# Kernel optimization log

Measured on AMD Instinct MI355X. Metric: run time of the kernel, lower is better.

## Reference

```python
import jax, jax.numpy as jnp
import numpy as np

N, C, NIRR, E = 2048, 128, 9, 10          # nodes, channels, sum(2l+1) of input irreps, num elements
DOUT = (1, 3)                              # output irrep dims for 128x0e + 128x1o
K3, K2, K1 = 4, 3, 2                       # number of CG paths per correlation order


def setup_inputs() -> dict:
    key = jax.random.key(0)
    ks = jax.random.split(key, 24)
    inp = {
        'node_feats': jax.random.normal(ks[0], (N, C, NIRR), jnp.float32),
        'node_attrs': jax.nn.one_hot(jax.random.randint(ks[1], (N,), 0, E), E, dtype=jnp.float32),
        'sc': jax.random.normal(ks[2], (N, C * sum(DOUT)), jnp.float32),
    }
    i = 3
    for li, d in enumerate(DOUT):
        # U tensors: fixed (buffer) generalized CG coupling tensors; sparse in e3nn,
        # here random dense stand-ins with the exact same shapes / contraction structure.
        inp[f'u3_l{li}'] = 0.1 * jax.random.normal(ks[i + 0], (d, NIRR, NIRR, NIRR, K3), jnp.float32)
        inp[f'u2_l{li}'] = 0.1 * jax.random.normal(ks[i + 1], (d, NIRR, NIRR, K2), jnp.float32)
        inp[f'u1_l{li}'] = 0.1 * jax.random.normal(ks[i + 2], (d, NIRR, K1), jnp.float32)
        s3, s2, s1 = 1.0 / np.sqrt(K3 * C), 1.0 / np.sqrt(K2 * C), 1.0 / np.sqrt(K1 * C)
        inp[f'w3_l{li}'] = s3 * jax.random.normal(ks[i + 3], (E, K3, C), jnp.float32)
        inp[f'w2_l{li}'] = s2 * jax.random.normal(ks[i + 4], (E, K2, C), jnp.float32)
        inp[f'w1_l{li}'] = s1 * jax.random.normal(ks[i + 5], (E, K1, C), jnp.float32)
        i += 6
    inp['lin_w0'] = jax.random.normal(ks[i], (C, C), jnp.float32)
    inp['lin_w1'] = jax.random.normal(ks[i + 1], (C, C), jnp.float32)
    return inp


def _contraction(x, y, u3, u2, u1, w3, w2, w1):
    # MACE Contraction: correlation-3 nested CG contraction for one output irrep.
    # x: [N,C,n], y: [N,E] one-hot, u_nu: [d, n*nu, k_nu], w_nu: [E, k_nu, C]
    wk3 = jnp.einsum('ekc,be->bkc', w3, y)                       # per-node path weights
    out = jnp.einsum('dpqik,bkc,bci->bcdpq', u3, wk3, x)         # main, nu=3
    out = jnp.einsum('dpik,ekc,be->bcdpi', u2, w2, y) + out      # add nu=2 weights
    out = jnp.einsum('bcdpi,bci->bcdp', out, x)                  # contract one feature index
    out = jnp.einsum('dik,ekc,be->bcdi', u1, w1, y) + out        # add nu=1 weights
    out = jnp.einsum('bcdi,bci->bcd', out, x)                    # [N,C,d]
    return out


def reference(node_feats, node_attrs, sc,
              u3_l0, u2_l0, u1_l0, w3_l0, w2_l0, w1_l0,
              u3_l1, u2_l1, u1_l1, w3_l1, w2_l1, w1_l1,
              lin_w0, lin_w1):
    f0 = _contraction(node_feats, node_attrs, u3_l0, u2_l0, u1_l0, w3_l0, w2_l0, w1_l0)  # [N,C,1]
    f1 = _contraction(node_feats, node_attrs, u3_l1, u2_l1, u1_l1, w3_l1, w2_l1, w1_l1)  # [N,C,3]
    inv_sqrt_c = 1.0 / np.sqrt(C).astype(np.float32)
    # o3.Linear: block-diagonal channel mixing per irrep, 1/sqrt(fan_in) normalization
    o0 = jnp.einsum('bim,ij->bjm', f0, lin_w0) * inv_sqrt_c
    o1 = jnp.einsum('bim,ij->bjm', f1, lin_w1) * inv_sqrt_c
    out = jnp.concatenate([o0.reshape(o0.shape[0], -1), o1.reshape(o1.shape[0], -1)], axis=-1)
    return out + sc
```

## Files before the change

kernel.cpp:

```cpp
#include <hip/hip_runtime.h>

#define N_NODES 2048
#define C_CH    128
#define NIRR    9
#define E_EL    10

#define NS3 165
#define NS2 45
#define US3_FLOATS (NS3 * 16)
#define US2_FLOATS (NS2 * 12)
#define US1_FLOATS (9 * 8)

struct Tab {
    unsigned char pairP[NS2], pairQ[NS2];
    unsigned char triPair[NS3], triI[NS3];
};
constexpr Tab makeTab() {
    Tab t{};
    int s2 = 0, s3 = 0;
    for (int p = 0; p < 9; p++)
        for (int q = p; q < 9; q++) {
            t.pairP[s2] = (unsigned char)p;
            t.pairQ[s2] = (unsigned char)q;
            for (int i = q; i < 9; i++) {
                t.triPair[s3] = (unsigned char)s2;
                t.triI[s3] = (unsigned char)i;
                s3++;
            }
            s2++;
        }
    return t;
}
constexpr Tab TAB = makeTab();

__global__ __launch_bounds__(256) void build_sym_kernel(
    const float* __restrict__ u3_l0, const float* __restrict__ u2_l0, const float* __restrict__ u1_l0,
    const float* __restrict__ u3_l1, const float* __restrict__ u2_l1, const float* __restrict__ u1_l1,
    float* __restrict__ us3, float* __restrict__ us2, float* __restrict__ us1)
{
    int t = blockIdx.x * 256 + threadIdx.x;
    if (t < US3_FLOATS) {
        int s = t >> 4, dk = t & 15, ds = dk >> 2, k = dk & 3;
        int pp = 0, qq = 0, ii = 0, cntr = 0;
        for (int p = 0; p < 9; p++)
            for (int q = p; q < 9; q++)
                for (int i = q; i < 9; i++) {
                    if (cntr == s) { pp = p; qq = q; ii = i; }
                    cntr++;
                }
        const float* u = (ds == 0) ? u3_l0 : (u3_l1 + (ds - 1) * 2916);
        int perm[6][3] = {{pp,qq,ii},{pp,ii,qq},{qq,pp,ii},{qq,ii,pp},{ii,pp,qq},{ii,qq,pp}};
        float acc = 0.f;
        #pragma unroll
        for (int j = 0; j < 6; j++)
            acc += u[((perm[j][0] * 9 + perm[j][1]) * 9 + perm[j][2]) * 4 + k];
        float mult = (pp == qq && qq == ii) ? 6.f : ((pp == qq || qq == ii) ? 2.f : 1.f);
        us3[ds * (NS3 * 4) + s * 4 + k] = acc / mult;
    } else if (t < US3_FLOATS + US2_FLOATS) {
        int t2 = t - US3_FLOATS;
        int s = t2 / 12, dk = t2 % 12, ds = dk / 3, k = dk % 3;
        int pp = 0, qq = 0, cntr = 0;
        for (int p = 0; p < 9; p++)
            for (int q = p; q < 9; q++) {
                if (cntr == s) { pp = p; qq = q; }
                cntr++;
            }
        const float* u = (ds == 0) ? u2_l0 : (u2_l1 + (ds - 1) * 243);
        float acc = u[(pp * 9 + qq) * 3 + k] + u[(qq * 9 + pp) * 3 + k];
        us2[ds * (NS2 * 3) + s * 3 + k] = (pp == qq) ? acc * 0.5f : acc;
    } else if (t < US3_FLOATS + US2_FLOATS + US1_FLOATS) {
        int t1 = t - US3_FLOATS - US2_FLOATS;
        int p = t1 >> 3, dk = t1 & 7, ds = dk >> 1, k = dk & 1;
        const float* u = (ds == 0) ? u1_l0 : (u1_l1 + (ds - 1) * 18);
        us1[ds * 18 + p * 2 + k] = u[p * 2 + k];
    }
}

__global__ __launch_bounds__(512, 4) void fused_kernel(
    const float* __restrict__ x, const float* __restrict__ y,
    const float* __restrict__ us3, const float* __restrict__ us2, const float* __restrict__ us1,
    const float* __restrict__ w3_l0, const float* __restrict__ w2_l0, const float* __restrict__ w1_l0,
    const float* __restrict__ w3_l1, const float* __restrict__ w2_l1, const float* __restrict__ w1_l1,
    const float* __restrict__ lw0, const float* __restrict__ lw1,
    const float* __restrict__ sc, float* __restrict__ out)
{
    __shared__ float fs[4][132];
    int tid = threadIdx.x;
    int c = tid & 127;
    int r = __builtin_amdgcn_readfirstlane(tid >> 7);
    int b = blockIdx.x;

    int e = 0;
    #pragma unroll
    for (int k = 1; k < E_EL; k++)
        if (y[b * E_EL + k] > 0.5f) e = k;
    e = __builtin_amdgcn_readfirstlane(e);

    float xv[9];
    {
        const float* xp = x + ((size_t)b * C_CH + c) * NIRR;
        #pragma unroll
        for (int i = 0; i < 9; i++) xv[i] = xp[i];
    }

    const float* t3 = us3 + r * (NS3 * 4);
    const float* t2 = us2 + r * (NS2 * 3);
    const float* t1 = us1 + r * 18;

    float G3[4] = {0.f, 0.f, 0.f, 0.f};
    float G2[3] = {0.f, 0.f, 0.f};
    float G1[2] = {0.f, 0.f};

    #pragma unroll
    for (int p = 0; p < 9; p++) {
        G1[0] += t1[p * 2 + 0] * xv[p];
        G1[1] += t1[p * 2 + 1] * xv[p];
    }

    float pq = 0.f;
    #pragma unroll
    for (int s = 0; s < NS3; s++) {
        const int pi = TAB.triPair[s];
        if (s == 0 || TAB.triPair[s] != TAB.triPair[s - 1]) {
            pq = xv[TAB.pairP[pi]] * xv[TAB.pairQ[pi]];
            G2[0] += t2[pi * 3 + 0] * pq;
            G2[1] += t2[pi * 3 + 1] * pq;
            G2[2] += t2[pi * 3 + 2] * pq;
        }
        float X = pq * xv[TAB.triI[s]];
        G3[0] += t3[s * 4 + 0] * X;
        G3[1] += t3[s * 4 + 1] * X;
        G3[2] += t3[s * 4 + 2] * X;
        G3[3] += t3[s * 4 + 3] * X;
    }

    float acc = 0.f;
    if (r == 0) {
        #pragma unroll
        for (int k = 0; k < 4; k++) acc += w3_l0[(e * 4 + k) * 128 + c] * G3[k];
        #pragma unroll
        for (int k = 0; k < 3; k++) acc += w2_l0[(e * 3 + k) * 128 + c] * G2[k];
        #pragma unroll
        for (int k = 0; k < 2; k++) acc += w1_l0[(e * 2 + k) * 128 + c] * G1[k];
    } else {
        #pragma unroll
        for (int k = 0; k < 4; k++) acc += w3_l1[(e * 4 + k) * 128 + c] * G3[k];
        #pragma unroll
        for (int k = 0; k < 3; k++) acc += w2_l1[(e * 3 + k) * 128 + c] * G2[k];
        #pragma unroll
        for (int k = 0; k < 2; k++) acc += w1_l1[(e * 2 + k) * 128 + c] * G1[k];
    }
    fs[r][c] = acc;
    __syncthreads();

    int sel, j, col;
    const float* W;
    if (tid < 128) { sel = 0; j = tid; col = tid; W = lw0; }
    else {
        int u = tid - 128;
        int m = u >> 7;
        j = u & 127;
        sel = 1 + m;
        col = 128 + 3 * j + m;
        W = lw1;
    }
    sel = __builtin_amdgcn_readfirstlane(sel);

    float a = 0.f;
    #pragma unroll 8
    for (int ib = 0; ib < 32; ib++) {
        float4 f = *(const float4*)&fs[sel][4 * ib];
        int i0 = 4 * ib;
        a += f.x * W[(i0 + 0) * 128 + j];
        a += f.y * W[(i0 + 1) * 128 + j];
        a += f.z * W[(i0 + 2) * 128 + j];
        a += f.w * W[(i0 + 3) * 128 + j];
    }

    const float inv_sqrt_c = 0.08838834764831845f;
    size_t oi = (size_t)b * 512 + col;
    out[oi] = a * inv_sqrt_c + sc[oi];
}

extern "C" void kernel_launch(void* const* d_in, const int* in_sizes, int n_in,
                              void* d_out, int out_size, void* d_ws, size_t ws_size,
                              hipStream_t stream) {
    const float* x     = (const float*)d_in[0];
    const float* y     = (const float*)d_in[1];
    const float* sc    = (const float*)d_in[2];
    const float* u3_l0 = (const float*)d_in[3];
    const float* u2_l0 = (const float*)d_in[4];
    const float* u1_l0 = (const float*)d_in[5];
    const float* w3_l0 = (const float*)d_in[6];
    const float* w2_l0 = (const float*)d_in[7];
    const float* w1_l0 = (const float*)d_in[8];
    const float* u3_l1 = (const float*)d_in[9];
    const float* u2_l1 = (const float*)d_in[10];
    const float* u1_l1 = (const float*)d_in[11];
    const float* w3_l1 = (const float*)d_in[12];
    const float* w2_l1 = (const float*)d_in[13];
    const float* w1_l1 = (const float*)d_in[14];
    const float* lw0   = (const float*)d_in[15];
    const float* lw1   = (const float*)d_in[16];
    float* out = (float*)d_out;

    float* us3 = (float*)d_ws;
    float* us2 = us3 + US3_FLOATS;
    float* us1 = us2 + US2_FLOATS;

    build_sym_kernel<<<13, 256, 0, stream>>>(
        u3_l0, u2_l0, u1_l0, u3_l1, u2_l1, u1_l1, us3, us2, us1);
    fused_kernel<<<N_NODES, 512, 0, stream>>>(
        x, y, us3, us2, us1,
        w3_l0, w2_l0, w1_l0, w3_l1, w2_l1, w1_l1,
        lw0, lw1, sc, out);
}
```

Before: 136.3 us.

## Fold symmetric CG table construction into main kernel via shared memory

Removes the separate table-building kernel and has every block rebuild the symmetrized U3/U2/U1 tables into LDS before the contraction. The U2 table is padded to four entries per row so the inner loop can use vectorized float4/float2 LDS reads. This saves one kernel launch and the global workspace round trip. In exchange, each block repeats the per-entry index search and permutation sums, and the coefficient reads move from uniform scalar loads to LDS loads.

```diff
diff --git a/kernel.cpp b/kernel.cpp
--- a/kernel.cpp
+++ b/kernel.cpp
@@ -7,9 +7,6 @@
 
 #define NS3 165
 #define NS2 45
-#define US3_FLOATS (NS3 * 16)
-#define US2_FLOATS (NS2 * 12)
-#define US1_FLOATS (9 * 8)
 
 struct Tab {
     unsigned char pairP[NS2], pairQ[NS2];
@@ -33,14 +30,27 @@
 }
 constexpr Tab TAB = makeTab();
 
-__global__ __launch_bounds__(256) void build_sym_kernel(
+__global__ __launch_bounds__(512, 4) void fused_kernel(
+    const float* __restrict__ x, const float* __restrict__ y,
     const float* __restrict__ u3_l0, const float* __restrict__ u2_l0, const float* __restrict__ u1_l0,
     const float* __restrict__ u3_l1, const float* __restrict__ u2_l1, const float* __restrict__ u1_l1,
-    float* __restrict__ us3, float* __restrict__ us2, float* __restrict__ us1)
+    const float* __restrict__ w3_l0, const float* __restrict__ w2_l0, const float* __restrict__ w1_l0,
+    const float* __restrict__ w3_l1, const float* __restrict__ w2_l1, const float* __restrict__ w1_l1,
+    const float* __restrict__ lw0, const float* __restrict__ lw1,
+    const float* __restrict__ sc, float* __restrict__ out)
 {
-    int t = blockIdx.x * 256 + threadIdx.x;
-    if (t < US3_FLOATS) {
-        int s = t >> 4, dk = t & 15, ds = dk >> 2, k = dk & 3;
+    __shared__ float lus3[4 * NS3 * 4];
+    __shared__ float lus2[4 * NS2 * 4];
+    __shared__ float lus1[4 * 9 * 2];
+    __shared__ float fs[4][132];
+
+    int tid = threadIdx.x;
+
+    for (int t = tid; t < 4 * NS3 * 4; t += 512) {
+        int k = t & 3;
+        int rs = t >> 2;
+        int s = rs % NS3;
+        int ds = rs / NS3;
         int pp = 0, qq = 0, ii = 0, cntr = 0;
         for (int p = 0; p < 9; p++)
             for (int q = p; q < 9; q++)
@@ -55,37 +65,36 @@
         for (int j = 0; j < 6; j++)
             acc += u[((perm[j][0] * 9 + perm[j][1]) * 9 + perm[j][2]) * 4 + k];
         float mult = (pp == qq && qq == ii) ? 6.f : ((pp == qq || qq == ii) ? 2.f : 1.f);
-        us3[ds * (NS3 * 4) + s * 4 + k] = acc / mult;
-    } else if (t < US3_FLOATS + US2_FLOATS) {
-        int t2 = t - US3_FLOATS;
-        int s = t2 / 12, dk = t2 % 12, ds = dk / 3, k = dk % 3;
-        int pp = 0, qq = 0, cntr = 0;
-        for (int p = 0; p < 9; p++)
-            for (int q = p; q < 9; q++) {
-                if (cntr == s) { pp = p; qq = q; }
-                cntr++;
-            }
-        const float* u = (ds == 0) ? u2_l0 : (u2_l1 + (ds - 1) * 243);
-        float acc = u[(pp * 9 + qq) * 3 + k] + u[(qq * 9 + pp) * 3 + k];
-        us2[ds * (NS2 * 3) + s * 3 + k] = (pp == qq) ? acc * 0.5f : acc;
-    } else if (t < US3_FLOATS + US2_FLOATS + US1_FLOATS) {
-        int t1 = t - US3_FLOATS - US2_FLOATS;
-        int p = t1 >> 3, dk = t1 & 7, ds = dk >> 1, k = dk & 1;
+        lus3[t] = acc / mult;
+    }
+    for (int t = tid; t < 4 * NS2 * 4; t += 512) {
+        int k = t & 3;
+        int rs = t >> 2;
+        int s = rs % NS2;
+        int ds = rs / NS2;
+        float v = 0.f;
+        if (k < 3) {
+            int pp = 0, qq = 0, cntr = 0;
+            for (int p = 0; p < 9; p++)
+                for (int q = p; q < 9; q++) {
+                    if (cntr == s) { pp = p; qq = q; }
+                    cntr++;
+                }
+            const float* u = (ds == 0) ? u2_l0 : (u2_l1 + (ds - 1) * 243);
+            float acc = u[(pp * 9 + qq) * 3 + k] + u[(qq * 9 + pp) * 3 + k];
+            v = (pp == qq) ? acc * 0.5f : acc;
+        }
+        lus2[t] = v;
+    }
+    if (tid < 72) {
+        int k = tid & 1;
+        int rp = tid >> 1;
+        int p = rp % 9;
+        int ds = rp / 9;
         const float* u = (ds == 0) ? u1_l0 : (u1_l1 + (ds - 1) * 18);
-        us1[ds * 18 + p * 2 + k] = u[p * 2 + k];
-    }
-}
-
-__global__ __launch_bounds__(512, 4) void fused_kernel(
-    const float* __restrict__ x, const float* __restrict__ y,
-    const float* __restrict__ us3, const float* __restrict__ us2, const float* __restrict__ us1,
-    const float* __restrict__ w3_l0, const float* __restrict__ w2_l0, const float* __restrict__ w1_l0,
-    const float* __restrict__ w3_l1, const float* __restrict__ w2_l1, const float* __restrict__ w1_l1,
-    const float* __restrict__ lw0, const float* __restrict__ lw1,
-    const float* __restrict__ sc, float* __restrict__ out)
-{
-    __shared__ float fs[4][132];
-    int tid = threadIdx.x;
+        lus1[tid] = u[p * 2 + k];
+    }
+
     int c = tid & 127;
     int r = __builtin_amdgcn_readfirstlane(tid >> 7);
     int b = blockIdx.x;
@@ -103,9 +112,11 @@
         for (int i = 0; i < 9; i++) xv[i] = xp[i];
     }
 
-    const float* t3 = us3 + r * (NS3 * 4);
-    const float* t2 = us2 + r * (NS2 * 3);
-    const float* t1 = us1 + r * 18;
+    __syncthreads();
+
+    const float* T3 = lus3 + r * (NS3 * 4);
+    const float* T2 = lus2 + r * (NS2 * 4);
+    const float* T1 = lus1 + r * 18;
 
     float G3[4] = {0.f, 0.f, 0.f, 0.f};
     float G2[3] = {0.f, 0.f, 0.f};
@@ -113,8 +124,9 @@
 
     #pragma unroll
     for (int p = 0; p < 9; p++) {
-        G1[0] += t1[p * 2 + 0] * xv[p];
-        G1[1] += t1[p * 2 + 1] * xv[p];
+        float2 u1v = *(const float2*)(T1 + p * 2);
+        G1[0] += u1v.x * xv[p];
+        G1[1] += u1v.y * xv[p];
     }
 
     float pq = 0.f;
@@ -123,15 +135,17 @@
         const int pi = TAB.triPair[s];
         if (s == 0 || TAB.triPair[s] != TAB.triPair[s - 1]) {
             pq = xv[TAB.pairP[pi]] * xv[TAB.pairQ[pi]];
-            G2[0] += t2[pi * 3 + 0] * pq;
-            G2[1] += t2[pi * 3 + 1] * pq;
-            G2[2] += t2[pi * 3 + 2] * pq;
+            float4 u2v = *(const float4*)(T2 + pi * 4);
+            G2[0] += u2v.x * pq;
+            G2[1] += u2v.y * pq;
+            G2[2] += u2v.z * pq;
         }
         float X = pq * xv[TAB.triI[s]];
-        G3[0] += t3[s * 4 + 0] * X;
-        G3[1] += t3[s * 4 + 1] * X;
-        G3[2] += t3[s * 4 + 2] * X;
-        G3[3] += t3[s * 4 + 3] * X;
+        float4 u3v = *(const float4*)(T3 + s * 4);
+        G3[0] += u3v.x * X;
+        G3[1] += u3v.y * X;
+        G3[2] += u3v.z * X;
+        G3[3] += u3v.w * X;
     }
 
     float acc = 0.f;
@@ -204,14 +218,9 @@
     const float* lw1   = (const float*)d_in[16];
     float* out = (float*)d_out;
 
-    float* us3 = (float*)d_ws;
-    float* us2 = us3 + US3_FLOATS;
-    float* us1 = us2 + US2_FLOATS;
-
-    build_sym_kernel<<<13, 256, 0, stream>>>(
-        u3_l0, u2_l0, u1_l0, u3_l1, u2_l1, u1_l1, us3, us2, us1);
     fused_kernel<<<N_NODES, 512, 0, stream>>>(
-        x, y, us3, us2, us1,
+        x, y,
+        u3_l0, u2_l0, u1_l0, u3_l1, u2_l1, u1_l1,
         w3_l0, w2_l0, w1_l0, w3_l1, w2_l1, w1_l1,
         lw0, lw1, sc, out);
 }
```

Result: slower. 190.2 us (+39.5%).
